# Kernel optimization log

Measured on AMD Instinct MI355X. Metric: run time of the kernel, lower is better.

Reference implementation:

```python
import jax, jax.numpy as jnp
import numpy as np

B, C, H = 64, 64, 32

def _pm_cross_pairs(ks):
    # Replicates PM_cross(2, ks): pairs (i, i+j) ordered by gap j=1..ks-1, then i.
    a, b = [], []
    for j in range(1, ks):
        for i in range(ks - j):
            a.append(i)
            b.append(i + j)
    return np.array(a, dtype=np.int32), np.array(b, dtype=np.int32)

def setup_inputs() -> dict:
    key = jax.random.key(0)
    k1, k2 = jax.random.split(key)
    ia, ib = _pm_cross_pairs(H)           # 496 pairs for H=32
    hk = ia.shape[0] + 2 * H              # 560
    x = jax.random.normal(k1, (B, C, H, H), dtype=jnp.float32)
    weight = 0.1 * jax.random.normal(k2, (C, H, hk, H), dtype=jnp.float32)
    return {"x": x, "weight": weight, "idx_a": jnp.asarray(ia), "idx_b": jnp.asarray(ib)}

def reference(x, weight, idx_a, idx_b):
    # cross-term products along last axis: [B,C,H,P]
    cross = x[..., idx_a] * x[..., idx_b]
    feat = jnp.concatenate([x, x * x, cross], axis=-1)  # [B,C,H,Hk]
    # per-(channel,row) grouped matmul
    return jnp.einsum('bcij,cijo->bcio', feat, weight)
```

## Files before the change

kernel.cpp:

```cpp
#include <hip/hip_runtime.h>

#define NB 64
#define NC 64
#define NH 32
#define HK 560
#define KPAD 576

typedef __bf16 bf16x8 __attribute__((ext_vector_type(8)));
typedef float f32x4 __attribute__((ext_vector_type(4)));

__device__ __forceinline__ unsigned short f2bf(float f) {
    unsigned u = __builtin_bit_cast(unsigned, f);
    u = (u + 0x7fffu + ((u >> 16) & 1u)) >> 16;
    return (unsigned short)u;
}

__global__ __launch_bounds__(256, 4) void hconv_kernel(
    const float* __restrict__ x, const float* __restrict__ w,
    const int* __restrict__ idx_a, const int* __restrict__ idx_b,
    float* __restrict__ out)
{
    __shared__ float s_x[NB][34];
    __shared__ unsigned s_lut[KPAD];
    __shared__ __align__(16) unsigned short s_feat[NB][72];
    __shared__ __align__(16) unsigned short s_wT[32][72];

    const int t = threadIdx.x;
    const int g = blockIdx.x;
    const int c = g >> 5, i = g & 31;

    {
        const int row = t >> 3;
        const int c4 = (t & 7) * 4;
        const float* xr = x + (((size_t)row * NC + c) * NH + i) * NH;
        const float* xr2 = xr + (size_t)32 * NC * NH * NH;
        float4 v = *(const float4*)(xr + c4);
        float4 v2 = *(const float4*)(xr2 + c4);
        s_x[row][c4] = v.x;  s_x[row][c4 + 1] = v.y;
        s_x[row][c4 + 2] = v.z; s_x[row][c4 + 3] = v.w;
        s_x[row + 32][c4] = v2.x;  s_x[row + 32][c4 + 1] = v2.y;
        s_x[row + 32][c4 + 2] = v2.z; s_x[row + 32][c4 + 3] = v2.w;
        if ((t & 7) == 0) {
            s_x[row][32] = 1.0f;      s_x[row][33] = 0.0f;
            s_x[row + 32][32] = 1.0f; s_x[row + 32][33] = 0.0f;
        }
    }

    for (int k = t; k < KPAD; k += 256) {
        unsigned pa, pb;
        if (k < 32)        { pa = (unsigned)k;        pb = 32u; }
        else if (k < 64)   { pa = (unsigned)(k - 32); pb = pa;  }
        else if (k < HK)   { pa = (unsigned)idx_a[k - 64]; pb = (unsigned)idx_b[k - 64]; }
        else               { pa = 33u; pb = 33u; }
        s_lut[k] = pa | (pb << 16);
    }

    const int wv = t >> 6;
    const int lane = t & 63;
    const int lr = lane & 15;
    const int lq = lane >> 4;
    const int fb = t >> 2;
    const int fq = t & 3;
    const int wo = t & 31;
    const int wkg = t >> 5;

    const float* wbase = w + (size_t)(c * NH + i) * HK * NH;

    f32x4 acc0 = {0.f, 0.f, 0.f, 0.f};
    f32x4 acc1 = {0.f, 0.f, 0.f, 0.f};

    for (int ch = 0; ch < 9; ++ch) {
        const int k0 = ch * 64;
        __syncthreads();

        {
            float v[8];
            const int kb = k0 + wkg * 8;
            #pragma unroll
            for (int r = 0; r < 8; ++r) {
                const int k = kb + r;
                v[r] = (k < HK) ? wbase[(size_t)k * NH + wo] : 0.0f;
            }
            uint4 pk;
            pk.x = (unsigned)f2bf(v[0]) | ((unsigned)f2bf(v[1]) << 16);
            pk.y = (unsigned)f2bf(v[2]) | ((unsigned)f2bf(v[3]) << 16);
            pk.z = (unsigned)f2bf(v[4]) | ((unsigned)f2bf(v[5]) << 16);
            pk.w = (unsigned)f2bf(v[6]) | ((unsigned)f2bf(v[7]) << 16);
            *(uint4*)&s_wT[wo][wkg * 8] = pk;
        }

        {
            unsigned pk[8];
            #pragma unroll
            for (int m = 0; m < 8; ++m) {
                const int kk = k0 + fq * 16 + 2 * m;
                const unsigned l0 = s_lut[kk], l1 = s_lut[kk + 1];
                const float p0 = s_x[fb][l0 & 0xffffu] * s_x[fb][l0 >> 16];
                const float p1 = s_x[fb][l1 & 0xffffu] * s_x[fb][l1 >> 16];
                pk[m] = (unsigned)f2bf(p0) | ((unsigned)f2bf(p1) << 16);
            }
            uint4 lo, hi;
            lo.x = pk[0]; lo.y = pk[1]; lo.z = pk[2]; lo.w = pk[3];
            hi.x = pk[4]; hi.y = pk[5]; hi.z = pk[6]; hi.w = pk[7];
            *(uint4*)&s_feat[fb][fq * 16] = lo;
            *(uint4*)&s_feat[fb][fq * 16 + 8] = hi;
        }

        __syncthreads();

        #pragma unroll
        for (int ks = 0; ks < 2; ++ks) {
            bf16x8 a  = *(const bf16x8*)&s_feat[wv * 16 + lr][ks * 32 + lq * 8];
            bf16x8 b0 = *(const bf16x8*)&s_wT[lr][ks * 32 + lq * 8];
            bf16x8 b1 = *(const bf16x8*)&s_wT[16 + lr][ks * 32 + lq * 8];
            acc0 = __builtin_amdgcn_mfma_f32_16x16x32_bf16(a, b0, acc0, 0, 0, 0);
            acc1 = __builtin_amdgcn_mfma_f32_16x16x32_bf16(a, b1, acc1, 0, 0, 0);
        }
    }

    #pragma unroll
    for (int r = 0; r < 4; ++r) {
        const int b = wv * 16 + lq * 4 + r;
        float* op = out + (((size_t)b * NC + c) * NH + i) * NH;
        op[lr] = acc0[r];
        op[16 + lr] = acc1[r];
    }
}

extern "C" void kernel_launch(void* const* d_in, const int* in_sizes, int n_in,
                              void* d_out, int out_size, void* d_ws, size_t ws_size,
                              hipStream_t stream) {
    const float* x = (const float*)d_in[0];
    const float* w = (const float*)d_in[1];
    const int* idx_a = (const int*)d_in[2];
    const int* idx_b = (const int*)d_in[3];
    float* out = (float*)d_out;
    hconv_kernel<<<dim3(NC * NH), dim3(256), 0, stream>>>(x, w, idx_a, idx_b, out);
}
```

Baseline: 233.2 us.

## Double-buffer weight tiles and build bf16 features directly in MFMA registers

Weights are now prefetched into registers one chunk ahead and written to a second shared-memory buffer after the MFMAs, leaving a single barrier per chunk instead of two. The feature tile in shared memory is removed: each lane computes its own A-fragment products from s_x through the LUT and converts them to bf16 in registers. Manual round-to-nearest-even is replaced by the native __bf16 cast. The aim is to hide global weight-load latency and cut LDS traffic and barriers, at the cost of more registers and some duplicated product work across lanes.

```diff
diff --git a/kernel.cpp b/kernel.cpp
--- a/kernel.cpp
+++ b/kernel.cpp
@@ -9,21 +9,14 @@
 typedef __bf16 bf16x8 __attribute__((ext_vector_type(8)));
 typedef float f32x4 __attribute__((ext_vector_type(4)));
 
-__device__ __forceinline__ unsigned short f2bf(float f) {
-    unsigned u = __builtin_bit_cast(unsigned, f);
-    u = (u + 0x7fffu + ((u >> 16) & 1u)) >> 16;
-    return (unsigned short)u;
-}
-
 __global__ __launch_bounds__(256, 4) void hconv_kernel(
     const float* __restrict__ x, const float* __restrict__ w,
     const int* __restrict__ idx_a, const int* __restrict__ idx_b,
     float* __restrict__ out)
 {
     __shared__ float s_x[NB][34];
-    __shared__ unsigned s_lut[KPAD];
-    __shared__ __align__(16) unsigned short s_feat[NB][72];
-    __shared__ __align__(16) unsigned short s_wT[32][72];
+    __shared__ __align__(16) unsigned s_lut[KPAD];
+    __shared__ __align__(16) unsigned short s_wT[2][32][72];
 
     const int t = threadIdx.x;
     const int g = blockIdx.x;
@@ -59,63 +52,64 @@
     const int lane = t & 63;
     const int lr = lane & 15;
     const int lq = lane >> 4;
-    const int fb = t >> 2;
-    const int fq = t & 3;
+    const int row = wv * 16 + lr;
     const int wo = t & 31;
     const int wkg = t >> 5;
 
     const float* wbase = w + (size_t)(c * NH + i) * HK * NH;
+
+    float pv[8];
+    #pragma unroll
+    for (int r = 0; r < 8; ++r)
+        pv[r] = wbase[(size_t)(wkg * 8 + r) * NH + wo];
+    {
+        bf16x8 wv8;
+        #pragma unroll
+        for (int r = 0; r < 8; ++r) wv8[r] = (__bf16)pv[r];
+        *(bf16x8*)&s_wT[0][wo][wkg * 8] = wv8;
+    }
+    __syncthreads();
 
     f32x4 acc0 = {0.f, 0.f, 0.f, 0.f};
     f32x4 acc1 = {0.f, 0.f, 0.f, 0.f};
 
     for (int ch = 0; ch < 9; ++ch) {
         const int k0 = ch * 64;
-        __syncthreads();
+        const int buf = ch & 1;
 
-        {
-            float v[8];
-            const int kb = k0 + wkg * 8;
+        if (ch < 8) {
+            const int kb = k0 + 64 + wkg * 8;
             #pragma unroll
             for (int r = 0; r < 8; ++r) {
                 const int k = kb + r;
-                v[r] = (k < HK) ? wbase[(size_t)k * NH + wo] : 0.0f;
+                pv[r] = (k < HK) ? wbase[(size_t)k * NH + wo] : 0.0f;
             }
-            uint4 pk;
-            pk.x = (unsigned)f2bf(v[0]) | ((unsigned)f2bf(v[1]) << 16);
-            pk.y = (unsigned)f2bf(v[2]) | ((unsigned)f2bf(v[3]) << 16);
-            pk.z = (unsigned)f2bf(v[4]) | ((unsigned)f2bf(v[5]) << 16);
-            pk.w = (unsigned)f2bf(v[6]) | ((unsigned)f2bf(v[7]) << 16);
-            *(uint4*)&s_wT[wo][wkg * 8] = pk;
         }
-
-        {
-            unsigned pk[8];
-            #pragma unroll
-            for (int m = 0; m < 8; ++m) {
-                const int kk = k0 + fq * 16 + 2 * m;
-                const unsigned l0 = s_lut[kk], l1 = s_lut[kk + 1];
-                const float p0 = s_x[fb][l0 & 0xffffu] * s_x[fb][l0 >> 16];
-                const float p1 = s_x[fb][l1 & 0xffffu] * s_x[fb][l1 >> 16];
-                pk[m] = (unsigned)f2bf(p0) | ((unsigned)f2bf(p1) << 16);
-            }
-            uint4 lo, hi;
-            lo.x = pk[0]; lo.y = pk[1]; lo.z = pk[2]; lo.w = pk[3];
-            hi.x = pk[4]; hi.y = pk[5]; hi.z = pk[6]; hi.w = pk[7];
-            *(uint4*)&s_feat[fb][fq * 16] = lo;
-            *(uint4*)&s_feat[fb][fq * 16 + 8] = hi;
-        }
-
-        __syncthreads();
 
         #pragma unroll
         for (int ks = 0; ks < 2; ++ks) {
-            bf16x8 a  = *(const bf16x8*)&s_feat[wv * 16 + lr][ks * 32 + lq * 8];
-            bf16x8 b0 = *(const bf16x8*)&s_wT[lr][ks * 32 + lq * 8];
-            bf16x8 b1 = *(const bf16x8*)&s_wT[16 + lr][ks * 32 + lq * 8];
+            const uint4* lp = (const uint4*)&s_lut[k0 + ks * 32 + lq * 8];
+            const uint4 L0 = lp[0], L1 = lp[1];
+            const unsigned pr[8] = {L0.x, L0.y, L0.z, L0.w, L1.x, L1.y, L1.z, L1.w};
+            bf16x8 a;
+            #pragma unroll
+            for (int j = 0; j < 8; ++j) {
+                const float p = s_x[row][pr[j] & 0xffffu] * s_x[row][pr[j] >> 16];
+                a[j] = (__bf16)p;
+            }
+            bf16x8 b0 = *(const bf16x8*)&s_wT[buf][lr][ks * 32 + lq * 8];
+            bf16x8 b1 = *(const bf16x8*)&s_wT[buf][16 + lr][ks * 32 + lq * 8];
             acc0 = __builtin_amdgcn_mfma_f32_16x16x32_bf16(a, b0, acc0, 0, 0, 0);
             acc1 = __builtin_amdgcn_mfma_f32_16x16x32_bf16(a, b1, acc1, 0, 0, 0);
         }
+
+        if (ch < 8) {
+            bf16x8 wv8;
+            #pragma unroll
+            for (int r = 0; r < 8; ++r) wv8[r] = (__bf16)pv[r];
+            *(bf16x8*)&s_wT[buf ^ 1][wo][wkg * 8] = wv8;
+        }
+        __syncthreads();
     }
 
     #pragma unroll
```

After: 238.8 us. 1.02x slower.
